# Performance work log

Hardware: AMD Instinct MI355X
Metric: run time of the kernel (lower is better)

## Reference

```python
import jax, jax.numpy as jnp
import numpy as np

N = 262144
D = 512
H = 512
G = 1024


def setup_inputs() -> dict:
    key = jax.random.key(0)
    k1, k2, k3, k4 = jax.random.split(key, 4)
    embed = jax.random.normal(k1, (N, D), dtype=jnp.float32)
    batch_index = jnp.sort(jax.random.randint(k2, (N,), 0, G)).astype(jnp.int64)
    # nn.Linear weights: W_att [atten_hidden, embed_size], V_att [1, atten_hidden]
    W_att = jax.random.normal(k3, (H, D), dtype=jnp.float32) * (1.0 / np.sqrt(D))
    V_att = jax.random.normal(k4, (1, H), dtype=jnp.float32) * (1.0 / np.sqrt(H))
    return {"embed": embed, "batch_index": batch_index, "W_att": W_att, "V_att": V_att, "num_segments": G}


def reference(embed, batch_index, W_att, V_att, num_segments):
    # beta = V(tanh(W(embed))).squeeze(-1)  -> [N]
    beta = jnp.einsum('nh,oh->no', jnp.tanh(jnp.einsum('nd,hd->nh', embed, W_att)), V_att).squeeze(-1)
    # segment softmax (unnormalized exp, as in the original module)
    exp_beta = jnp.exp(beta)
    grouped_sum = jax.ops.segment_sum(exp_beta, batch_index, num_segments=num_segments)  # [G]
    alpha = exp_beta / grouped_sum[batch_index]  # [N]
    # scatter-weighted sum of node embeddings per graph -> [G, D]
    result = jax.ops.segment_sum(alpha[:, None] * embed, batch_index, num_segments=num_segments)
    return result
```

## Files before the change

### kernel.cpp

```cpp
#include <hip/hip_runtime.h>
#include <hip/hip_bf16.h>

#define D_DIM 512
#define H_DIM 512
#define G_SEG 1024
#define BM    64

typedef __attribute__((ext_vector_type(8))) short bf16x8;
typedef __attribute__((ext_vector_type(4))) float f32x4;
typedef unsigned int u32;
typedef unsigned short u16;

#define WS_S   0
#define WS_WB  8192

#define AS_BYTES  (BM * 1024)
#define BETA_OFF  AS_BYTES
#define EBS_OFF   (BETA_OFF + 4 * BM * 4)
#define SIDX_OFF  (EBS_OFF + BM * 4)
#define SCR_OFF   (SIDX_OFF + BM * 4)
#define LDS_TOTAL (SCR_OFF + 4 * 512 * 4)

static __device__ __forceinline__ u16 f2bf(float f) {
    __hip_bfloat16 h = __float2bfloat16(f);
    return *(u16*)&h;
}
static __device__ __forceinline__ float bf2f(u16 u) {
    return __uint_as_float(((u32)u) << 16);
}
static __device__ __forceinline__ float fast_tanh(float x) {
    float e = exp2f(x * 2.885390081777927f);
    return 1.0f - 2.0f * __builtin_amdgcn_rcpf(e + 1.0f);
}
static __device__ __forceinline__ void pack8(const float4& a, const float4& b, void* dst) {
    u16 h[8];
    h[0]=f2bf(a.x); h[1]=f2bf(a.y); h[2]=f2bf(a.z); h[3]=f2bf(a.w);
    h[4]=f2bf(b.x); h[5]=f2bf(b.y); h[6]=f2bf(b.z); h[7]=f2bf(b.w);
    *(uint4*)dst = *(uint4*)h;
}

__global__ __launch_bounds__(256)
void cvt_w(const float* __restrict__ W, u16* __restrict__ Wb) {
    int t   = blockIdx.x * 256 + threadIdx.x;
    int lhi = t & 3;
    int c   = (t >> 2) & 511;
    int k32 = t >> 11;
    const float* src = W + (size_t)c * 512 + k32 * 32 + lhi * 8;
    float4 f0 = *(const float4*)(src);
    float4 f1 = *(const float4*)(src + 4);
    pack8(f0, f1, Wb + (size_t)t * 8);
}

__global__ __launch_bounds__(256, 2)
void fused(const float* __restrict__ E, const int* __restrict__ BI,
           const u16* __restrict__ Wb, const float* __restrict__ V,
           float* __restrict__ out, float* __restrict__ S)
{
    extern __shared__ char smem[];
    const int tid = threadIdx.x;
    const int nodeBase = blockIdx.x * BM;
    const int l   = tid & 63;
    const int w   = tid >> 6;
    const int l15 = l & 15;
    const int lhi = l >> 4;

    const float* Eb = E + (size_t)nodeBase * 512;

    {
        const int rbase0 = w * 16;
        float4 LA[8], LB[8];
        auto loadRound = [&](int p, float4* L) {
#pragma unroll
            for (int i = 0; i < 8; ++i) {
                int row  = rbase0 + p * 4 + (i >> 1);
                int half = i & 1;
                L[i] = *(const float4*)(Eb + (size_t)row * 512 + half * 256 + l * 4);
            }
        };
        auto writeRound = [&](int p, float4* L) {
#pragma unroll
            for (int i = 0; i < 8; ++i) {
                int row  = rbase0 + p * 4 + (i >> 1);
                int half = i & 1;
                int g16  = half * 32 + (l >> 1);
                int byte = row * 1024 + ((g16 * 16) ^ ((row & 7) << 4)) + (l & 1) * 8;
                u16 h[4];
                h[0] = f2bf(L[i].x); h[1] = f2bf(L[i].y);
                h[2] = f2bf(L[i].z); h[3] = f2bf(L[i].w);
                *(uint2*)(smem + byte) = *(uint2*)h;
            }
        };
        loadRound(0, LA);
        loadRound(1, LB);
        writeRound(0, LA);
        loadRound(2, LA);
        writeRound(1, LB);
        loadRound(3, LB);
        writeRound(2, LA);
        writeRound(3, LB);
    }
    __syncthreads();

    f32x4 acc[4][8];
#pragma unroll
    for (int m = 0; m < 4; ++m)
#pragma unroll
        for (int n = 0; n < 8; ++n) acc[m][n] = (f32x4){0.f, 0.f, 0.f, 0.f};

    const int bOffBase = ((w * 128 + l15) * 4 + lhi) * 16;
    const char* Wbb = (const char*)Wb;

    bf16x8 bA[8], bB[8];
#pragma unroll
    for (int n = 0; n < 8; ++n)
        bA[n] = *(const bf16x8*)(Wbb + bOffBase + n * 1024);

#pragma unroll 1
    for (int kk2 = 0; kk2 < 8; ++kk2) {
        {
            const char* Wn = Wbb + ((size_t)(2 * kk2 + 1) << 15);
#pragma unroll
            for (int n = 0; n < 8; ++n)
                bB[n] = *(const bf16x8*)(Wn + bOffBase + n * 1024);
            bf16x8 a[4];
            const int kbyte = (2 * kk2) * 64 + lhi * 16;
#pragma unroll
            for (int m = 0; m < 4; ++m) {
                int row = m * 16 + l15;
                a[m] = *(const bf16x8*)(smem + row * 1024 + (kbyte ^ ((row & 7) << 4)));
            }
#pragma unroll
            for (int m = 0; m < 4; ++m)
#pragma unroll
                for (int n = 0; n < 8; ++n)
                    acc[m][n] = __builtin_amdgcn_mfma_f32_16x16x32_bf16(a[m], bA[n], acc[m][n], 0, 0, 0);
        }
        {
            if (kk2 < 7) {
                const char* Wn = Wbb + ((size_t)(2 * kk2 + 2) << 15);
#pragma unroll
                for (int n = 0; n < 8; ++n)
                    bA[n] = *(const bf16x8*)(Wn + bOffBase + n * 1024);
            }
            bf16x8 a[4];
            const int kbyte = (2 * kk2 + 1) * 64 + lhi * 16;
#pragma unroll
            for (int m = 0; m < 4; ++m) {
                int row = m * 16 + l15;
                a[m] = *(const bf16x8*)(smem + row * 1024 + (kbyte ^ ((row & 7) << 4)));
            }
#pragma unroll
            for (int m = 0; m < 4; ++m)
#pragma unroll
                for (int n = 0; n < 8; ++n)
                    acc[m][n] = __builtin_amdgcn_mfma_f32_16x16x32_bf16(a[m], bB[n], acc[m][n], 0, 0, 0);
        }
    }

    float Vv[8];
#pragma unroll
    for (int n = 0; n < 8; ++n)
        Vv[n] = V[w * 128 + n * 16 + l15];

    float bsum[4][4];
#pragma unroll
    for (int m = 0; m < 4; ++m)
#pragma unroll
        for (int r = 0; r < 4; ++r) {
            float s = 0.f;
#pragma unroll
            for (int n = 0; n < 8; ++n)
                s += Vv[n] * fast_tanh(acc[m][n][r]);
            bsum[m][r] = s;
        }
#pragma unroll
    for (int off = 1; off <= 8; off <<= 1)
#pragma unroll
        for (int m = 0; m < 4; ++m)
#pragma unroll
            for (int r = 0; r < 4; ++r)
                bsum[m][r] += __shfl_xor(bsum[m][r], off, 64);

    float* betaP = (float*)(smem + BETA_OFF);
    if (l15 == 0) {
#pragma unroll
        for (int m = 0; m < 4; ++m)
#pragma unroll
            for (int r = 0; r < 4; ++r)
                betaP[w * BM + m * 16 + lhi * 4 + r] = bsum[m][r];
    }
    __syncthreads();

    float* ebs  = (float*)(smem + EBS_OFF);
    int*   sidx = (int*)(smem + SIDX_OFF);
    if (tid < BM) {
        float beta = betaP[tid] + betaP[BM + tid] + betaP[2 * BM + tid] + betaP[3 * BM + tid];
        float eb = expf(beta);
        ebs[tid] = eb;
        int g = BI[nodeBase + tid];
        sidx[tid] = g;
        int g0 = __shfl(g, 0, 64);
        if (__all(g == g0)) {
            float s = eb;
#pragma unroll
            for (int off = 1; off <= 32; off <<= 1)
                s += __shfl_xor(s, off, 64);
            if (l == 0) atomicAdd(&S[g], s);
        } else {
            atomicAdd(&S[g], eb);
        }
    }
    __syncthreads();

    {
        float* scr = (float*)(smem + SCR_OFF) + w * 512;
        const int rbase = w * 16;
        float a8[8];
#pragma unroll
        for (int j = 0; j < 8; ++j) a8[j] = 0.f;
        int gcur = sidx[rbase];

#pragma unroll 1
        for (int rr = 0; rr < 16; ++rr) {
            int r = rbase + rr;
            int g = sidx[r];
            if (g != gcur) {
                *(float4*)(scr + l * 8)     = make_float4(a8[0], a8[1], a8[2], a8[3]);
                *(float4*)(scr + l * 8 + 4) = make_float4(a8[4], a8[5], a8[6], a8[7]);
                asm volatile("s_waitcnt lgkmcnt(0)" ::: "memory");
#pragma unroll
                for (int j = 0; j < 8; ++j)
                    atomicAdd(&out[(size_t)gcur * 512 + j * 64 + l], scr[j * 64 + l]);
#pragma unroll
                for (int j = 0; j < 8; ++j) a8[j] = 0.f;
                gcur = g;
            }
            float wgt = ebs[r];
            bf16x8 v = *(const bf16x8*)(smem + r * 1024 + ((l * 16) ^ ((r & 7) << 4)));
#pragma unroll
            for (int j = 0; j < 8; ++j)
                a8[j] += wgt * bf2f((u16)v[j]);
        }
        *(float4*)(scr + l * 8)     = make_float4(a8[0], a8[1], a8[2], a8[3]);
        *(float4*)(scr + l * 8 + 4) = make_float4(a8[4], a8[5], a8[6], a8[7]);
        asm volatile("s_waitcnt lgkmcnt(0)" ::: "memory");
#pragma unroll
        for (int j = 0; j < 8; ++j)
            atomicAdd(&out[(size_t)gcur * 512 + j * 64 + l], scr[j * 64 + l]);
    }
}

__global__ __launch_bounds__(256)
void finalize_kernel(float* __restrict__ out, const float* __restrict__ S) {
    int idx = blockIdx.x * 256 + threadIdx.x;
    float s = S[idx >> 9];
    float v = out[idx];
    out[idx] = (s != 0.f) ? v * __builtin_amdgcn_rcpf(s) : 0.f;
}

extern "C" void kernel_launch(void* const* d_in, const int* in_sizes, int n_in,
                              void* d_out, int out_size, void* d_ws, size_t ws_size,
                              hipStream_t stream) {
    const float* E  = (const float*)d_in[0];
    const int*   BI = (const int*)d_in[1];
    const float* W  = (const float*)d_in[2];
    const float* V  = (const float*)d_in[3];
    float* out = (float*)d_out;
    char*  ws  = (char*)d_ws;
    const int Ntot = in_sizes[0] / D_DIM;

    float* S  = (float*)(ws + WS_S);
    u16*   Wb = (u16*)(ws + WS_WB);

    hipMemsetAsync(S, 0, G_SEG * 4, stream);
    hipMemsetAsync(out, 0, (size_t)out_size * 4, stream);
    hipFuncSetAttribute((const void*)fused,
                        hipFuncAttributeMaxDynamicSharedMemorySize, LDS_TOTAL);

    cvt_w<<<128, 256, 0, stream>>>(W, Wb);
    fused<<<Ntot / BM, 256, LDS_TOTAL, stream>>>(E, BI, Wb, V, out, S);
    finalize_kernel<<<out_size / 256, 256, 0, stream>>>(out, S);
}
```

Baseline: 351.9 us.

## Make fused kernel persistent over tiles with double-buffered embed prefetch

Each block now handles eight consecutive 64-node tiles. While the current tile runs its MFMA, epilogue and scatter phases, the next tile's fp32 embed rows are loaded from global memory and written as bf16 into a second LDS buffer, so load latency overlaps compute. The grid shrinks eightfold and launch bounds drop to one block per CU because LDS use doubles. Fewer resident blocks may reduce latency hiding and leave CUs unevenly loaded.

```diff
diff --git a/kernel.cpp b/kernel.cpp
--- a/kernel.cpp
+++ b/kernel.cpp
@@ -5,6 +5,7 @@
 #define H_DIM 512
 #define G_SEG 1024
 #define BM    64
+#define TILES 8
 
 typedef __attribute__((ext_vector_type(8))) short bf16x8;
 typedef __attribute__((ext_vector_type(4))) float f32x4;
@@ -14,8 +15,9 @@
 #define WS_S   0
 #define WS_WB  8192
 
-#define AS_BYTES  (BM * 1024)
-#define BETA_OFF  AS_BYTES
+#define BUF0_OFF  0
+#define BUF1_OFF  (BM * 1024)
+#define BETA_OFF  (2 * BM * 1024)
 #define EBS_OFF   (BETA_OFF + 4 * BM * 4)
 #define SIDX_OFF  (EBS_OFF + BM * 4)
 #define SCR_OFF   (SIDX_OFF + BM * 4)
@@ -32,11 +34,10 @@
     float e = exp2f(x * 2.885390081777927f);
     return 1.0f - 2.0f * __builtin_amdgcn_rcpf(e + 1.0f);
 }
-static __device__ __forceinline__ void pack8(const float4& a, const float4& b, void* dst) {
-    u16 h[8];
-    h[0]=f2bf(a.x); h[1]=f2bf(a.y); h[2]=f2bf(a.z); h[3]=f2bf(a.w);
-    h[4]=f2bf(b.x); h[5]=f2bf(b.y); h[6]=f2bf(b.z); h[7]=f2bf(b.w);
-    *(uint4*)dst = *(uint4*)h;
+static __device__ __forceinline__ void barrier_lds() {
+    asm volatile("s_waitcnt lgkmcnt(0)" ::: "memory");
+    __builtin_amdgcn_s_barrier();
+    __builtin_amdgcn_sched_barrier(0);
 }
 
 __global__ __launch_bounds__(256)
@@ -48,205 +49,234 @@
     const float* src = W + (size_t)c * 512 + k32 * 32 + lhi * 8;
     float4 f0 = *(const float4*)(src);
     float4 f1 = *(const float4*)(src + 4);
-    pack8(f0, f1, Wb + (size_t)t * 8);
-}
-
-__global__ __launch_bounds__(256, 2)
+    u16 h[8];
+    h[0]=f2bf(f0.x); h[1]=f2bf(f0.y); h[2]=f2bf(f0.z); h[3]=f2bf(f0.w);
+    h[4]=f2bf(f1.x); h[5]=f2bf(f1.y); h[6]=f2bf(f1.z); h[7]=f2bf(f1.w);
+    *(uint4*)(Wb + (size_t)t * 8) = *(uint4*)h;
+}
+
+__global__ __launch_bounds__(256, 1)
 void fused(const float* __restrict__ E, const int* __restrict__ BI,
            const u16* __restrict__ Wb, const float* __restrict__ V,
            float* __restrict__ out, float* __restrict__ S)
 {
     extern __shared__ char smem[];
     const int tid = threadIdx.x;
-    const int nodeBase = blockIdx.x * BM;
     const int l   = tid & 63;
     const int w   = tid >> 6;
     const int l15 = l & 15;
     const int lhi = l >> 4;
-
-    const float* Eb = E + (size_t)nodeBase * 512;
-
-    {
-        const int rbase0 = w * 16;
-        float4 LA[8], LB[8];
-        auto loadRound = [&](int p, float4* L) {
-#pragma unroll
-            for (int i = 0; i < 8; ++i) {
-                int row  = rbase0 + p * 4 + (i >> 1);
-                int half = i & 1;
-                L[i] = *(const float4*)(Eb + (size_t)row * 512 + half * 256 + l * 4);
-            }
-        };
-        auto writeRound = [&](int p, float4* L) {
-#pragma unroll
-            for (int i = 0; i < 8; ++i) {
-                int row  = rbase0 + p * 4 + (i >> 1);
-                int half = i & 1;
-                int g16  = half * 32 + (l >> 1);
-                int byte = row * 1024 + ((g16 * 16) ^ ((row & 7) << 4)) + (l & 1) * 8;
-                u16 h[4];
-                h[0] = f2bf(L[i].x); h[1] = f2bf(L[i].y);
-                h[2] = f2bf(L[i].z); h[3] = f2bf(L[i].w);
-                *(uint2*)(smem + byte) = *(uint2*)h;
-            }
-        };
-        loadRound(0, LA);
-        loadRound(1, LB);
-        writeRound(0, LA);
-        loadRound(2, LA);
-        writeRound(1, LB);
-        loadRound(3, LB);
-        writeRound(2, LA);
-        writeRound(3, LB);
-    }
-    __syncthreads();
-
-    f32x4 acc[4][8];
-#pragma unroll
-    for (int m = 0; m < 4; ++m)
-#pragma unroll
-        for (int n = 0; n < 8; ++n) acc[m][n] = (f32x4){0.f, 0.f, 0.f, 0.f};
+    const int tile0 = blockIdx.x * TILES;
 
     const int bOffBase = ((w * 128 + l15) * 4 + lhi) * 16;
     const char* Wbb = (const char*)Wb;
 
+    float4 LA[8], LB[8];
+    auto issueB = [&](int gTile, int p, float4* L) {
+        const float* Eb = E + (size_t)gTile * (BM * 512);
+#pragma unroll
+        for (int i = 0; i < 8; ++i) {
+            int row  = w * 16 + p * 4 + (i >> 1);
+            int half = i & 1;
+            L[i] = *(const float4*)(Eb + (size_t)row * 512 + half * 256 + l * 4);
+        }
+    };
+    auto writeB = [&](char* buf, int p, float4* L) {
+#pragma unroll
+        for (int i = 0; i < 8; ++i) {
+            int row  = w * 16 + p * 4 + (i >> 1);
+            int half = i & 1;
+            int g16  = half * 32 + (l >> 1);
+            int byte = row * 1024 + ((g16 * 16) ^ ((row & 7) << 4)) + (l & 1) * 8;
+            u16 h[4];
+            h[0] = f2bf(L[i].x); h[1] = f2bf(L[i].y);
+            h[2] = f2bf(L[i].z); h[3] = f2bf(L[i].w);
+            *(uint2*)(buf + byte) = *(uint2*)h;
+        }
+    };
+
+    issueB(tile0, 0, LA);
+    issueB(tile0, 1, LB);
+    writeB(smem + BUF0_OFF, 0, LA);
+    issueB(tile0, 2, LA);
+    writeB(smem + BUF0_OFF, 1, LB);
+    issueB(tile0, 3, LB);
+    writeB(smem + BUF0_OFF, 2, LA);
+    writeB(smem + BUF0_OFF, 3, LB);
+    barrier_lds();
+
     bf16x8 bA[8], bB[8];
 #pragma unroll
     for (int n = 0; n < 8; ++n)
         bA[n] = *(const bf16x8*)(Wbb + bOffBase + n * 1024);
 
+    int cur = 0;
 #pragma unroll 1
-    for (int kk2 = 0; kk2 < 8; ++kk2) {
+    for (int t = 0; t < TILES; ++t) {
+        char* bufC = smem + (cur ? BUF1_OFF : BUF0_OFF);
+        char* bufN = smem + (cur ? BUF0_OFF : BUF1_OFF);
+        const bool more  = (t + 1 < TILES);
+        const int  tNext = tile0 + t + 1;
+        const int  nodeBase = (tile0 + t) * BM;
+
+        f32x4 acc[4][8];
+#pragma unroll
+        for (int m = 0; m < 4; ++m)
+#pragma unroll
+            for (int n = 0; n < 8; ++n) acc[m][n] = (f32x4){0.f, 0.f, 0.f, 0.f};
+
+#pragma unroll 1
+        for (int kk2 = 0; kk2 < 8; ++kk2) {
+            if (more && kk2 == 0) issueB(tNext, 0, LA);
+            if (more && kk2 == 2) issueB(tNext, 1, LB);
+            if (more && kk2 == 5) writeB(bufN, 0, LA);
+            if (more && kk2 == 7) writeB(bufN, 1, LB);
+            {
+                const char* Wn = Wbb + ((size_t)(2 * kk2 + 1) << 15);
+#pragma unroll
+                for (int n = 0; n < 8; ++n)
+                    bB[n] = *(const bf16x8*)(Wn + bOffBase + n * 1024);
+                bf16x8 a[4];
+                const int kbyte = (2 * kk2) * 64 + lhi * 16;
+#pragma unroll
+                for (int m = 0; m < 4; ++m) {
+                    int row = m * 16 + l15;
+                    a[m] = *(const bf16x8*)(bufC + row * 1024 + (kbyte ^ ((row & 7) << 4)));
+                }
+#pragma unroll
+                for (int m = 0; m < 4; ++m)
+#pragma unroll
+                    for (int n = 0; n < 8; ++n)
+                        acc[m][n] = __builtin_amdgcn_mfma_f32_16x16x32_bf16(a[m], bA[n], acc[m][n], 0, 0, 0);
+            }
+            {
+                if (kk2 < 7) {
+                    const char* Wn = Wbb + ((size_t)(2 * kk2 + 2) << 15);
+#pragma unroll
+                    for (int n = 0; n < 8; ++n)
+                        bA[n] = *(const bf16x8*)(Wn + bOffBase + n * 1024);
+                }
+                bf16x8 a[4];
+                const int kbyte = (2 * kk2 + 1) * 64 + lhi * 16;
+#pragma unroll
+                for (int m = 0; m < 4; ++m) {
+                    int row = m * 16 + l15;
+                    a[m] = *(const bf16x8*)(bufC + row * 1024 + (kbyte ^ ((row & 7) << 4)));
+                }
+#pragma unroll
+                for (int m = 0; m < 4; ++m)
+#pragma unroll
+                    for (int n = 0; n < 8; ++n)
+                        acc[m][n] = __builtin_amdgcn_mfma_f32_16x16x32_bf16(a[m], bB[n], acc[m][n], 0, 0, 0);
+            }
+        }
+
+        if (more) issueB(tNext, 2, LA);
+        if (more) {
+#pragma unroll
+            for (int n = 0; n < 8; ++n)
+                bA[n] = *(const bf16x8*)(Wbb + bOffBase + n * 1024);
+        }
+
+        float Vv[8];
+#pragma unroll
+        for (int n = 0; n < 8; ++n)
+            Vv[n] = V[w * 128 + n * 16 + l15];
+
+        float bsum[4][4];
+#pragma unroll
+        for (int m = 0; m < 4; ++m)
+#pragma unroll
+            for (int r = 0; r < 4; ++r) {
+                float s = 0.f;
+#pragma unroll
+                for (int n = 0; n < 8; ++n)
+                    s += Vv[n] * fast_tanh(acc[m][n][r]);
+                bsum[m][r] = s;
+            }
+#pragma unroll
+        for (int off = 1; off <= 8; off <<= 1)
+#pragma unroll
+            for (int m = 0; m < 4; ++m)
+#pragma unroll
+                for (int r = 0; r < 4; ++r)
+                    bsum[m][r] += __shfl_xor(bsum[m][r], off, 64);
+
+        if (more) writeB(bufN, 2, LA);
+
+        float* betaP = (float*)(smem + BETA_OFF);
+        if (l15 == 0) {
+#pragma unroll
+            for (int m = 0; m < 4; ++m)
+#pragma unroll
+                for (int r = 0; r < 4; ++r)
+                    betaP[w * BM + m * 16 + lhi * 4 + r] = bsum[m][r];
+        }
+        barrier_lds();
+
+        if (more) issueB(tNext, 3, LB);
+
+        float* ebs  = (float*)(smem + EBS_OFF);
+        int*   sidx = (int*)(smem + SIDX_OFF);
+        if (tid < BM) {
+            float beta = betaP[tid] + betaP[BM + tid] + betaP[2 * BM + tid] + betaP[3 * BM + tid];
+            float eb = expf(beta);
+            ebs[tid] = eb;
+            int g = BI[nodeBase + tid];
+            sidx[tid] = g;
+            int g0 = __shfl(g, 0, 64);
+            if (__all(g == g0)) {
+                float s = eb;
+#pragma unroll
+                for (int off = 1; off <= 32; off <<= 1)
+                    s += __shfl_xor(s, off, 64);
+                if (l == 0) atomicAdd(&S[g], s);
+            } else {
+                atomicAdd(&S[g], eb);
+            }
+        }
+        barrier_lds();
+
         {
-            const char* Wn = Wbb + ((size_t)(2 * kk2 + 1) << 15);
-#pragma unroll
-            for (int n = 0; n < 8; ++n)
-                bB[n] = *(const bf16x8*)(Wn + bOffBase + n * 1024);
-            bf16x8 a[4];
-            const int kbyte = (2 * kk2) * 64 + lhi * 16;
-#pragma unroll
-            for (int m = 0; m < 4; ++m) {
-                int row = m * 16 + l15;
-                a[m] = *(const bf16x8*)(smem + row * 1024 + (kbyte ^ ((row & 7) << 4)));
-            }
-#pragma unroll
-            for (int m = 0; m < 4; ++m)
-#pragma unroll
-                for (int n = 0; n < 8; ++n)
-                    acc[m][n] = __builtin_amdgcn_mfma_f32_16x16x32_bf16(a[m], bA[n], acc[m][n], 0, 0, 0);
-        }
-        {
-            if (kk2 < 7) {
-                const char* Wn = Wbb + ((size_t)(2 * kk2 + 2) << 15);
-#pragma unroll
-                for (int n = 0; n < 8; ++n)
-                    bA[n] = *(const bf16x8*)(Wn + bOffBase + n * 1024);
-            }
-            bf16x8 a[4];
-            const int kbyte = (2 * kk2 + 1) * 64 + lhi * 16;
-#pragma unroll
-            for (int m = 0; m < 4; ++m) {
-                int row = m * 16 + l15;
-                a[m] = *(const bf16x8*)(smem + row * 1024 + (kbyte ^ ((row & 7) << 4)));
-            }
-#pragma unroll
-            for (int m = 0; m < 4; ++m)
-#pragma unroll
-                for (int n = 0; n < 8; ++n)
-                    acc[m][n] = __builtin_amdgcn_mfma_f32_16x16x32_bf16(a[m], bB[n], acc[m][n], 0, 0, 0);
-        }
-    }
-
-    float Vv[8];
-#pragma unroll
-    for (int n = 0; n < 8; ++n)
-        Vv[n] = V[w * 128 + n * 16 + l15];
-
-    float bsum[4][4];
-#pragma unroll
-    for (int m = 0; m < 4; ++m)
-#pragma unroll
-        for (int r = 0; r < 4; ++r) {
-            float s = 0.f;
-#pragma unroll
-            for (int n = 0; n < 8; ++n)
-                s += Vv[n] * fast_tanh(acc[m][n][r]);
-            bsum[m][r] = s;
-        }
-#pragma unroll
-    for (int off = 1; off <= 8; off <<= 1)
-#pragma unroll
-        for (int m = 0; m < 4; ++m)
-#pragma unroll
-            for (int r = 0; r < 4; ++r)
-                bsum[m][r] += __shfl_xor(bsum[m][r], off, 64);
-
-    float* betaP = (float*)(smem + BETA_OFF);
-    if (l15 == 0) {
-#pragma unroll
-        for (int m = 0; m < 4; ++m)
-#pragma unroll
-            for (int r = 0; r < 4; ++r)
-                betaP[w * BM + m * 16 + lhi * 4 + r] = bsum[m][r];
-    }
-    __syncthreads();
-
-    float* ebs  = (float*)(smem + EBS_OFF);
-    int*   sidx = (int*)(smem + SIDX_OFF);
-    if (tid < BM) {
-        float beta = betaP[tid] + betaP[BM + tid] + betaP[2 * BM + tid] + betaP[3 * BM + tid];
-        float eb = expf(beta);
-        ebs[tid] = eb;
-        int g = BI[nodeBase + tid];
-        sidx[tid] = g;
-        int g0 = __shfl(g, 0, 64);
-        if (__all(g == g0)) {
-            float s = eb;
-#pragma unroll
-            for (int off = 1; off <= 32; off <<= 1)
-                s += __shfl_xor(s, off, 64);
-            if (l == 0) atomicAdd(&S[g], s);
-        } else {
-            atomicAdd(&S[g], eb);
-        }
-    }
-    __syncthreads();
-
-    {
-        float* scr = (float*)(smem + SCR_OFF) + w * 512;
-        const int rbase = w * 16;
-        float a8[8];
-#pragma unroll
-        for (int j = 0; j < 8; ++j) a8[j] = 0.f;
-        int gcur = sidx[rbase];
+            float* scr = (float*)(smem + SCR_OFF) + w * 512;
+            const int rbase = w * 16;
+            float a8[8];
+#pragma unroll
+            for (int j = 0; j < 8; ++j) a8[j] = 0.f;
+            int gcur = sidx[rbase];
 
 #pragma unroll 1
-        for (int rr = 0; rr < 16; ++rr) {
-            int r = rbase + rr;
-            int g = sidx[r];
-            if (g != gcur) {
-                *(float4*)(scr + l * 8)     = make_float4(a8[0], a8[1], a8[2], a8[3]);
-                *(float4*)(scr + l * 8 + 4) = make_float4(a8[4], a8[5], a8[6], a8[7]);
-                asm volatile("s_waitcnt lgkmcnt(0)" ::: "memory");
+            for (int rr = 0; rr < 16; ++rr) {
+                int r = rbase + rr;
+                int g = sidx[r];
+                if (g != gcur) {
+                    *(float4*)(scr + l * 8)     = make_float4(a8[0], a8[1], a8[2], a8[3]);
+                    *(float4*)(scr + l * 8 + 4) = make_float4(a8[4], a8[5], a8[6], a8[7]);
+                    asm volatile("s_waitcnt lgkmcnt(0)" ::: "memory");
+#pragma unroll
+                    for (int j = 0; j < 8; ++j)
+                        atomicAdd(&out[(size_t)gcur * 512 + j * 64 + l], scr[j * 64 + l]);
+#pragma unroll
+                    for (int j = 0; j < 8; ++j) a8[j] = 0.f;
+                    gcur = g;
+                }
+                float wgt = ebs[r];
+                bf16x8 v = *(const bf16x8*)(bufC + r * 1024 + ((l * 16) ^ ((r & 7) << 4)));
 #pragma unroll
                 for (int j = 0; j < 8; ++j)
-                    atomicAdd(&out[(size_t)gcur * 512 + j * 64 + l], scr[j * 64 + l]);
-#pragma unroll
-                for (int j = 0; j < 8; ++j) a8[j] = 0.f;
-                gcur = g;
-            }
-            float wgt = ebs[r];
-            bf16x8 v = *(const bf16x8*)(smem + r * 1024 + ((l * 16) ^ ((r & 7) << 4)));
+                    a8[j] += wgt * bf2f((u16)v[j]);
+            }
+            *(float4*)(scr + l * 8)     = make_float4(a8[0], a8[1], a8[2], a8[3]);
+            *(float4*)(scr + l * 8 + 4) = make_float4(a8[4], a8[5], a8[6], a8[7]);
+            asm volatile("s_waitcnt lgkmcnt(0)" ::: "memory");
 #pragma unroll
             for (int j = 0; j < 8; ++j)
-                a8[j] += wgt * bf2f((u16)v[j]);
-        }
-        *(float4*)(scr + l * 8)     = make_float4(a8[0], a8[1], a8[2], a8[3]);
-        *(float4*)(scr + l * 8 + 4) = make_float4(a8[4], a8[5], a8[6], a8[7]);
-        asm volatile("s_waitcnt lgkmcnt(0)" ::: "memory");
-#pragma unroll
-        for (int j = 0; j < 8; ++j)
-            atomicAdd(&out[(size_t)gcur * 512 + j * 64 + l], scr[j * 64 + l]);
+                atomicAdd(&out[(size_t)gcur * 512 + j * 64 + l], scr[j * 64 + l]);
+        }
+
+        if (more) writeB(bufN, 3, LB);
+        barrier_lds();
+        cur ^= 1;
     }
 }
 
@@ -278,6 +308,6 @@
                         hipFuncAttributeMaxDynamicSharedMemorySize, LDS_TOTAL);
 
     cvt_w<<<128, 256, 0, stream>>>(W, Wb);
-    fused<<<Ntot / BM, 256, LDS_TOTAL, stream>>>(E, BI, Wb, V, out, S);
+    fused<<<Ntot / (BM * TILES), 256, LDS_TOTAL, stream>>>(E, BI, Wb, V, out, S);
     finalize_kernel<<<out_size / 256, 256, 0, stream>>>(out, S);
 }
```

Result: no change. 346.9 us (-1.4%).
